# Optimization experiments

Measured on AMD Instinct MI355X. Metric: run time of the kernel, lower is better.

Reference implementation:

```python
import jax, jax.numpy as jnp
import numpy as np

K, D = 512, 64
B, H, W = 32, 64, 64


def setup_inputs() -> dict:
    key = jax.random.key(0)
    k1, k2 = jax.random.split(key)
    z_e_x = jax.random.normal(k1, (B, D, H, W), dtype=jnp.float32)
    # nn.Embedding weight initialized uniform(-1/K, 1/K)
    codebook = jax.random.uniform(k2, (K, D), dtype=jnp.float32,
                                  minval=-1.0 / K, maxval=1.0 / K)
    return {"z_e_x": z_e_x, "codebook": codebook}


def _quantize_indices(flat, codebook):
    # distances[n,k] = ||c_k||^2 + ||x_n||^2 - 2 x_n . c_k  (addmm form)
    cb_sqr = jnp.sum(codebook * codebook, axis=1)            # [K]
    x_sqr = jnp.sum(flat * flat, axis=1, keepdims=True)      # [N,1]
    distances = cb_sqr + x_sqr - 2.0 * (flat @ codebook.T)   # [N,K]
    return jnp.argmin(distances, axis=1)                     # [N]


def reference(z_e_x, codebook):
    # VQEmbedding.straight_through forward: returns (z_q_x, z_q_x_bar), both NCHW.
    b, d, h, w = z_e_x.shape
    x = jnp.transpose(z_e_x, (0, 2, 3, 1))       # NHWC
    flat = x.reshape(-1, d)                      # [N,D]
    idx = _quantize_indices(flat, codebook)      # [N]
    codes = jnp.take(codebook, idx, axis=0).reshape(b, h, w, d)
    z_q = jnp.transpose(codes, (0, 3, 1, 2))     # NCHW
    # z_q_x (detached codebook path) and z_q_x_bar (live codebook path) are
    # numerically identical in the forward pass.
    return (z_q, z_q)
```

## Files before the change

kernel.cpp:

```cpp
#include <hip/hip_runtime.h>


typedef short bf16x8 __attribute__((ext_vector_type(8)));
typedef float f32x4  __attribute__((ext_vector_type(4)));

#define KCODES 512
#define DDIM 64
#define HWSZ 4096
#define NPOS 131072
#define POSB 128
#define NBLK (NPOS / POSB)
#define OUT2_OFF 8388608
#define S_X 129

__device__ __forceinline__ unsigned short f2bf_rne(float f) {
    unsigned u = __builtin_bit_cast(unsigned, f);
    unsigned r = u + 0x7FFFu + ((u >> 16) & 1u);
    return (unsigned short)(r >> 16);
}
__device__ __forceinline__ float bf2f(unsigned short h) {
    unsigned u = ((unsigned)h) << 16;
    return __builtin_bit_cast(float, u);
}

__device__ __forceinline__ float np_sumsq64(const float* __restrict__ a) {
#pragma clang fp contract(off)
    float r0 = a[0]*a[0], r1 = a[1]*a[1], r2 = a[2]*a[2], r3 = a[3]*a[3];
    float r4 = a[4]*a[4], r5 = a[5]*a[5], r6 = a[6]*a[6], r7 = a[7]*a[7];
#pragma unroll
    for (int i = 8; i < 64; i += 8) {
        r0 += a[i+0]*a[i+0]; r1 += a[i+1]*a[i+1];
        r2 += a[i+2]*a[i+2]; r3 += a[i+3]*a[i+3];
        r4 += a[i+4]*a[i+4]; r5 += a[i+5]*a[i+5];
        r6 += a[i+6]*a[i+6]; r7 += a[i+7]*a[i+7];
    }
    return ((r0+r1)+(r2+r3)) + ((r4+r5)+(r6+r7));
}

__global__ __launch_bounds__(256) void vq_prep(
    const float* __restrict__ cb, unsigned short* __restrict__ wsb,
    float* __restrict__ wscb)
{
    if (blockIdx.x < 128) {
        int u = blockIdx.x * 256 + threadIdx.x;
        int k = u >> 6, d = u & 63;
        float c = cb[u];
        unsigned short ch = f2bf_rne(c);
        float clf = c - bf2f(ch);
        unsigned short cl = f2bf_rne(clf);
        int tile = k >> 4, n = k & 15;
        int chunk = d >> 5, quad = (d >> 3) & 3, j = d & 7;
        int lane = quad * 16 + n;
        size_t base = ((((size_t)tile*2 + chunk)*2 + 0)*64 + lane)*8 + j;
        wsb[base]       = (unsigned short)ch;
        wsb[base + 512] = (unsigned short)cl;
    } else {
        int k = (blockIdx.x - 128) * 256 + threadIdx.x;
        if (k < KCODES) wscb[k] = np_sumsq64(cb + k * DDIM);
    }
}

__global__ __launch_bounds__(256, 4) void vq_main(
    const float* __restrict__ z, const float* __restrict__ cb,
    const unsigned short* __restrict__ wsb, const float* __restrict__ wscb,
    float* __restrict__ out)
{
#pragma clang fp contract(off)
    __shared__ float s_regA[64 * S_X];
    __shared__ float s_cbsqr[KCODES];
    __shared__ float s_xsqr[POSB];
    __shared__ float s_part[2 * POSB];
    __shared__ int   s_idx[POSB];
    __shared__ int   s_flist[POSB];
    __shared__ int   s_cnt;

    const int tid = threadIdx.x;
    const int wv = tid >> 6, ln = tid & 63;
    const int m = ln & 15, q = ln >> 4;
    const int n0 = blockIdx.x * POSB;
    const long gbase = (long)(n0 >> 12) * (DDIM * HWSZ) + (n0 & 4095);

    if (tid == 0) s_cnt = 0;
    s_cbsqr[tid] = wscb[tid];
    s_cbsqr[tid + 256] = wscb[tid + 256];

#pragma unroll
    for (int i = 0; i < 32; ++i) {
        int d = wv * 16 + (i & 15), ph = i >> 4;
        s_regA[d * S_X + ph * 64 + ln] = z[gbase + (long)d * HWSZ + ph * 64 + ln];
    }
    __syncthreads();

    {
        int p = tid & 127, h = tid >> 7;
        float r0 = 0.f, r1 = 0.f, r2 = 0.f, r3 = 0.f;
#pragma unroll
        for (int i = 0; i < 8; ++i) {
            float a0 = s_regA[(8*i + 4*h + 0) * S_X + p];
            float a1 = s_regA[(8*i + 4*h + 1) * S_X + p];
            float a2 = s_regA[(8*i + 4*h + 2) * S_X + p];
            float a3 = s_regA[(8*i + 4*h + 3) * S_X + p];
            r0 += a0*a0; r1 += a1*a1; r2 += a2*a2; r3 += a3*a3;
        }
        s_part[h * POSB + p] = (r0 + r1) + (r2 + r3);
    }

    bf16x8 Ah[4], Al[4];
#pragma unroll
    for (int rt = 0; rt < 2; ++rt)
#pragma unroll
        for (int c = 0; c < 2; ++c) {
            int pos = wv * 32 + rt * 16 + m;
            bf16x8 ah, al;
#pragma unroll
            for (int j = 0; j < 8; ++j) {
                float xv = s_regA[(c*32 + q*8 + j) * S_X + pos];
                unsigned short hh = f2bf_rne(xv);
                float lo = xv - bf2f(hh);
                ah[j] = (short)hh;
                al[j] = (short)f2bf_rne(lo);
            }
            Ah[rt*2 + c] = ah; Al[rt*2 + c] = al;
        }
    __syncthreads();
    if (tid < POSB) s_xsqr[tid] = s_part[tid] + s_part[POSB + tid];

    float m1[8], m2[8]; int t1[8];
#pragma unroll
    for (int i = 0; i < 8; ++i) { m1[i] = 3.4e38f; m2[i] = 3.4e38f; t1[i] = 0; }

    for (int g = 0; g < 4; ++g) {
        __syncthreads();
        const float4* src = (const float4*)wsb + g * 2048;
        float4* dst = (float4*)s_regA;
#pragma unroll
        for (int i = 0; i < 8; ++i) dst[i * 256 + tid] = src[i * 256 + tid];
        __syncthreads();

        const unsigned short* sb = (const unsigned short*)s_regA;
        for (int ti = 0; ti < 8; ++ti) {
            int t = g * 8 + ti;
            bf16x8 Bh0 = *(const bf16x8*)(sb + ((ti*2+0)*2+0)*512 + ln*8);
            bf16x8 Bl0 = *(const bf16x8*)(sb + ((ti*2+0)*2+1)*512 + ln*8);
            bf16x8 Bh1 = *(const bf16x8*)(sb + ((ti*2+1)*2+0)*512 + ln*8);
            bf16x8 Bl1 = *(const bf16x8*)(sb + ((ti*2+1)*2+1)*512 + ln*8);
            float cbv = s_cbsqr[t * 16 + m];
#pragma unroll
            for (int rt = 0; rt < 2; ++rt) {
                f32x4 acc = {0.f, 0.f, 0.f, 0.f};
                acc = __builtin_amdgcn_mfma_f32_16x16x32_bf16(Al[rt*2+0], Bh0, acc, 0,0,0);
                acc = __builtin_amdgcn_mfma_f32_16x16x32_bf16(Ah[rt*2+0], Bl0, acc, 0,0,0);
                acc = __builtin_amdgcn_mfma_f32_16x16x32_bf16(Ah[rt*2+0], Bh0, acc, 0,0,0);
                acc = __builtin_amdgcn_mfma_f32_16x16x32_bf16(Al[rt*2+1], Bh1, acc, 0,0,0);
                acc = __builtin_amdgcn_mfma_f32_16x16x32_bf16(Ah[rt*2+1], Bl1, acc, 0,0,0);
                acc = __builtin_amdgcn_mfma_f32_16x16x32_bf16(Ah[rt*2+1], Bh1, acc, 0,0,0);
#pragma unroll
                for (int r = 0; r < 4; ++r) {
                    float sc = fmaf(-2.f, acc[r], cbv);
                    int cell = rt * 4 + r;
                    bool lt = sc < m1[cell];
                    m2[cell] = fminf(m2[cell], lt ? m1[cell] : sc);
                    if (lt) { m1[cell] = sc; t1[cell] = t; }
                }
            }
        }
    }

#pragma unroll
    for (int cell = 0; cell < 8; ++cell) {
        int rt = cell >> 2, r = cell & 3;
        float v1 = m1[cell], v2 = m2[cell];
        int i1 = t1[cell] * 16 + m;
#pragma unroll
        for (int s = 1; s < 16; s <<= 1) {
            float o1 = __shfl_xor(v1, s);
            float o2 = __shfl_xor(v2, s);
            int   oi = __shfl_xor(i1, s);
            bool take = (o1 < v1) || (o1 == v1 && oi < i1);
            float lose = take ? v1 : o1;
            if (take) { v1 = o1; i1 = oi; }
            v2 = fminf(fminf(v2, o2), lose);
        }
        if (m == 0) {
            int pos = wv * 32 + rt * 16 + q * 4 + r;
            float xs = s_xsqr[pos];
            float sx = 8.0f * sqrtf(xs) * 1.01f;
            float amax = 0.00196f * sx + 0.01f;
            float eps = 1.5f * (3.0f * 1.52587890625e-5f * 0.00196f * sx
                                + 500.f * 5.96e-8f * amax);
            float delta = 2.4e-7f * (xs + 1.0f) + 64.f * 1.2e-7f * amax;
            float W = 2.f * eps + 2.f * delta + 1e-9f;
            int flag = (v2 - v1 <= W) ? (1 << 30) : 0;
            s_idx[pos] = i1 | flag;
        }
    }
    __syncthreads();
    if (tid < POSB) {
        if (s_idx[tid] & (1 << 30)) {
            int slot = atomicAdd(&s_cnt, 1);
            s_flist[slot] = tid;
        }
    }
    __syncthreads();

    const int cnt = s_cnt;
    for (int i = wv; i < cnt; i += 4) {
        int p = __builtin_amdgcn_readfirstlane(s_flist[i]);
        float xv = z[gbase + (long)ln * HWSZ + p];
        float xs = s_xsqr[p];
        float dot[8];
#pragma unroll
        for (int j = 0; j < 8; ++j) dot[j] = 0.f;
        const float* crow = cb + (ln * 8) * DDIM;
        for (int dc = 0; dc < 16; ++dc) {
            float x0 = __shfl(xv, dc*4 + 0);
            float x1 = __shfl(xv, dc*4 + 1);
            float x2 = __shfl(xv, dc*4 + 2);
            float x3 = __shfl(xv, dc*4 + 3);
#pragma unroll
            for (int j = 0; j < 8; ++j) {
                float4 cv = *(const float4*)(crow + j * DDIM + dc * 4);
                dot[j] = fmaf(x0, cv.x, dot[j]);
                dot[j] = fmaf(x1, cv.y, dot[j]);
                dot[j] = fmaf(x2, cv.z, dot[j]);
                dot[j] = fmaf(x3, cv.w, dot[j]);
            }
        }
        float bv = 3.4e38f; int bi = 0;
#pragma unroll
        for (int j = 0; j < 8; ++j) {
            int k = ln * 8 + j;
            float tt = s_cbsqr[k] + xs;
            float e = fmaf(-2.f, dot[j], tt);
            if (e < bv) { bv = e; bi = k; }
        }
#pragma unroll
        for (int s = 1; s < 64; s <<= 1) {
            float ov = __shfl_xor(bv, s); int oi = __shfl_xor(bi, s);
            if (ov < bv || (ov == bv && oi < bi)) { bv = ov; bi = oi; }
        }
        if (ln == 0) s_idx[p] = bi;
    }
    __syncthreads();

    {
        int p = tid & 127, hf = tid >> 7;
        int idx = s_idx[p] & 0x3FFFFFFF;
        const float4* crow4 = (const float4*)(cb + idx * DDIM + hf * 32);
        float* o0 = out + gbase + p;
        float* o1 = o0 + OUT2_OFF;
#pragma unroll
        for (int qq = 0; qq < 8; ++qq) {
            float4 v = crow4[qq];
            long db = (long)(hf * 32 + qq * 4) * HWSZ;
            o0[db]          = v.x; o0[db + HWSZ]   = v.y;
            o0[db + 2*HWSZ] = v.z; o0[db + 3*HWSZ] = v.w;
            o1[db]          = v.x; o1[db + HWSZ]   = v.y;
            o1[db + 2*HWSZ] = v.z; o1[db + 3*HWSZ] = v.w;
        }
    }
}

extern "C" void kernel_launch(void* const* d_in, const int* in_sizes, int n_in,
                              void* d_out, int out_size, void* d_ws, size_t ws_size,
                              hipStream_t stream) {
    const float* z  = (const float*)d_in[0];
    const float* cb = (const float*)d_in[1];
    float* out = (float*)d_out;
    unsigned short* wsb = (unsigned short*)d_ws;
    float* wscb = (float*)((char*)d_ws + 131072);
    vq_prep<<<130, 256, 0, stream>>>(cb, wsb, wscb);
    vq_main<<<NBLK, 256, 0, stream>>>(z, cb, wsb, wscb, out);
}
```

Baseline: 178.9 us.

## Vectorize z loads and output stores via LDS staging, stream codebook from global

Loads the z tile with float4 global reads into a padded LDS buffer (stride 132), and stages gathered codebook rows in LDS so the two NCHW outputs are written with coalesced float4 stores. The codebook bf16 fragments are now read directly from global/L2 with one-tile register prefetch instead of being copied into LDS in four synchronized groups. The fallback exact path reads x from LDS rather than global memory. It trades LDS bank behaviour and global-load latency on the MFMA loop for fewer barriers and wider memory transactions.

Measured after the change: 157.5 us. -12.0%, faster.

```diff
diff --git a/kernel.cpp b/kernel.cpp
--- a/kernel.cpp
+++ b/kernel.cpp
@@ -11,7 +11,8 @@
 #define POSB 128
 #define NBLK (NPOS / POSB)
 #define OUT2_OFF 8388608
-#define S_X 129
+#define S_X 132
+#define S_X4 (S_X / 4)
 
 __device__ __forceinline__ unsigned short f2bf_rne(float f) {
     unsigned u = __builtin_bit_cast(unsigned, f);
@@ -66,13 +67,14 @@
     float* __restrict__ out)
 {
 #pragma clang fp contract(off)
-    __shared__ float s_regA[64 * S_X];
+    __shared__ float4 s_xbuf4[DDIM * S_X4];
     __shared__ float s_cbsqr[KCODES];
     __shared__ float s_xsqr[POSB];
     __shared__ float s_part[2 * POSB];
     __shared__ int   s_idx[POSB];
     __shared__ int   s_flist[POSB];
     __shared__ int   s_cnt;
+    float* s_regA = (float*)s_xbuf4;
 
     const int tid = threadIdx.x;
     const int wv = tid >> 6, ln = tid & 63;
@@ -84,10 +86,14 @@
     s_cbsqr[tid] = wscb[tid];
     s_cbsqr[tid + 256] = wscb[tid + 256];
 
-#pragma unroll
-    for (int i = 0; i < 32; ++i) {
-        int d = wv * 16 + (i & 15), ph = i >> 4;
-        s_regA[d * S_X + ph * 64 + ln] = z[gbase + (long)d * HWSZ + ph * 64 + ln];
+    {
+        const float4* z4 = (const float4*)(z + gbase);
+#pragma unroll
+        for (int i = 0; i < 8; ++i) {
+            int v = i * 256 + tid;
+            int d = v >> 5, p4 = v & 31;
+            s_xbuf4[d * S_X4 + p4] = z4[d * (HWSZ / 4) + p4];
+        }
     }
     __syncthreads();
 
@@ -124,26 +130,28 @@
         }
     __syncthreads();
     if (tid < POSB) s_xsqr[tid] = s_part[tid] + s_part[POSB + tid];
+    __syncthreads();
 
     float m1[8], m2[8]; int t1[8];
 #pragma unroll
     for (int i = 0; i < 8; ++i) { m1[i] = 3.4e38f; m2[i] = 3.4e38f; t1[i] = 0; }
 
-    for (int g = 0; g < 4; ++g) {
-        __syncthreads();
-        const float4* src = (const float4*)wsb + g * 2048;
-        float4* dst = (float4*)s_regA;
-#pragma unroll
-        for (int i = 0; i < 8; ++i) dst[i * 256 + tid] = src[i * 256 + tid];
-        __syncthreads();
-
-        const unsigned short* sb = (const unsigned short*)s_regA;
-        for (int ti = 0; ti < 8; ++ti) {
-            int t = g * 8 + ti;
-            bf16x8 Bh0 = *(const bf16x8*)(sb + ((ti*2+0)*2+0)*512 + ln*8);
-            bf16x8 Bl0 = *(const bf16x8*)(sb + ((ti*2+0)*2+1)*512 + ln*8);
-            bf16x8 Bh1 = *(const bf16x8*)(sb + ((ti*2+1)*2+0)*512 + ln*8);
-            bf16x8 Bl1 = *(const bf16x8*)(sb + ((ti*2+1)*2+1)*512 + ln*8);
+    {
+        const unsigned short* wbl = wsb + ln * 8;
+        bf16x8 pBh0 = *(const bf16x8*)(wbl + 0);
+        bf16x8 pBl0 = *(const bf16x8*)(wbl + 512);
+        bf16x8 pBh1 = *(const bf16x8*)(wbl + 1024);
+        bf16x8 pBl1 = *(const bf16x8*)(wbl + 1536);
+#pragma unroll 4
+        for (int t = 0; t < 32; ++t) {
+            bf16x8 Bh0 = pBh0, Bl0 = pBl0, Bh1 = pBh1, Bl1 = pBl1;
+            if (t < 31) {
+                const unsigned short* nb = wbl + (t + 1) * 2048;
+                pBh0 = *(const bf16x8*)(nb + 0);
+                pBl0 = *(const bf16x8*)(nb + 512);
+                pBh1 = *(const bf16x8*)(nb + 1024);
+                pBl1 = *(const bf16x8*)(nb + 1536);
+            }
             float cbv = s_cbsqr[t * 16 + m];
 #pragma unroll
             for (int rt = 0; rt < 2; ++rt) {
@@ -206,7 +214,7 @@
     const int cnt = s_cnt;
     for (int i = wv; i < cnt; i += 4) {
         int p = __builtin_amdgcn_readfirstlane(s_flist[i]);
-        float xv = z[gbase + (long)ln * HWSZ + p];
+        float xv = s_regA[ln * S_X + p];
         float xs = s_xsqr[p];
         float dot[8];
 #pragma unroll
@@ -247,16 +255,28 @@
         int p = tid & 127, hf = tid >> 7;
         int idx = s_idx[p] & 0x3FFFFFFF;
         const float4* crow4 = (const float4*)(cb + idx * DDIM + hf * 32);
-        float* o0 = out + gbase + p;
-        float* o1 = o0 + OUT2_OFF;
-#pragma unroll
-        for (int qq = 0; qq < 8; ++qq) {
-            float4 v = crow4[qq];
-            long db = (long)(hf * 32 + qq * 4) * HWSZ;
-            o0[db]          = v.x; o0[db + HWSZ]   = v.y;
-            o0[db + 2*HWSZ] = v.z; o0[db + 3*HWSZ] = v.w;
-            o1[db]          = v.x; o1[db + HWSZ]   = v.y;
-            o1[db + 2*HWSZ] = v.z; o1[db + 3*HWSZ] = v.w;
+#pragma unroll
+        for (int j4 = 0; j4 < 8; ++j4) {
+            float4 cv = crow4[j4];
+            int d = hf * 32 + j4 * 4;
+            s_regA[(d + 0) * S_X + p] = cv.x;
+            s_regA[(d + 1) * S_X + p] = cv.y;
+            s_regA[(d + 2) * S_X + p] = cv.z;
+            s_regA[(d + 3) * S_X + p] = cv.w;
+        }
+    }
+    __syncthreads();
+
+    {
+        float4* o4 = (float4*)(out + gbase);
+#pragma unroll
+        for (int i = 0; i < 8; ++i) {
+            int v = i * 256 + tid;
+            int d = v >> 5, p4 = v & 31;
+            float4 val = s_xbuf4[d * S_X4 + p4];
+            size_t off = (size_t)d * (HWSZ / 4) + p4;
+            o4[off] = val;
+            o4[off + (OUT2_OFF / 4)] = val;
         }
     }
 }
```
